# Kernel optimization log

Measured on AMD Instinct MI355X. Metric: run time of the kernel, lower is better.

Reference implementation:

```python
import jax, jax.numpy as jnp
import numpy as np

B, T, C, H = 8, 4096, 1024, 64

def setup_inputs() -> dict:
    key = jax.random.key(0)
    k1, k2, k3, k4 = jax.random.split(key, 4)
    return {
        "x": jax.random.normal(k1, (B, T, C), dtype=jnp.float32),
        "Wq": jax.random.normal(k2, (C, H), dtype=jnp.float32) * (C ** -0.5),
        "Wk": jax.random.normal(k3, (C, H), dtype=jnp.float32) * (C ** -0.5),
        "Wv": jax.random.normal(k4, (C, H), dtype=jnp.float32) * (C ** -0.5),
    }

def reference(x, Wq, Wk, Wv):
    # x: [B, T, C]; projections are bias-free Linears
    q = jnp.einsum("btc,ch->bth", x, Wq)  # [B, T, H]
    k = jnp.einsum("btc,ch->bth", x, Wk)
    v = jnp.einsum("btc,ch->bth", x, Wv)
    # NOTE: original scales by C**-0.5 (embed size), not head_size**-0.5
    scores = jnp.einsum("bqh,bkh->bqk", q, k) * (x.shape[-1] ** -0.5)  # [B, T, T]
    causal = jnp.tril(jnp.ones((x.shape[1], x.shape[1]), dtype=bool))
    scores = jnp.where(causal, scores, -jnp.inf)
    weights = jax.nn.softmax(scores, axis=-1)
    # dropout p=0.0 (eval) -> identity
    return jnp.einsum("bqk,bkh->bqh", weights, v)  # [B, T, H]
```

## Files before the change

### kernel.cpp

```cpp
#include <hip/hip_runtime.h>
#include <hip/hip_bf16.h>

typedef __attribute__((ext_vector_type(8))) short short8;
typedef __attribute__((ext_vector_type(4))) float f32x4;
typedef unsigned short u16;
typedef unsigned int u32;
typedef unsigned long long u64;

typedef u64    __attribute__((may_alias)) u64a;
typedef short8 __attribute__((may_alias)) short8a;
typedef float4 __attribute__((may_alias)) float4a;

#define Tseq 4096
#define LPP  72

__device__ __forceinline__ u32 pk_bf(float a, float b) {
    union { __hip_bfloat162 h; u32 u; } t;
    float2 f; f.x = a; f.y = b;
    t.h = __float22bfloat162_rn(f);
    return t.u;
}

__device__ __forceinline__ u16 f2bf(float f) {
    u32 u = __float_as_uint(f);
    u = (u + 0x7FFFu + ((u >> 16) & 1u)) >> 16;
    return (u16)u;
}

__device__ __forceinline__ short8 ld_frag_lds(const u16* p) {
    union { short8 v; u64 u[2]; } t;
    t.u[0] = *(const u64a*)(p);
    t.u[1] = *(const u64a*)(p + 4);
    return t.v;
}

__device__ __forceinline__ short8 cvt8(float4 a, float4 b) {
    union { short8 s; u32 u[4]; } t;
    t.u[0] = pk_bf(a.x, a.y); t.u[1] = pk_bf(a.z, a.w);
    t.u[2] = pk_bf(b.x, b.y); t.u[3] = pk_bf(b.z, b.w);
    return t.s;
}

__device__ __forceinline__ void gld_lds16(const void* g, void* l) {
    __builtin_amdgcn_global_load_lds(
        (const __attribute__((address_space(1))) u32*)g,
        (__attribute__((address_space(3))) u32*)l, 16, 0, 0);
}

__global__ __launch_bounds__(256) void wt_kernel(const float* __restrict__ Wq,
                                                 const float* __restrict__ Wk,
                                                 const float* __restrict__ Wv,
                                                 u16* __restrict__ wtf) {
    int idx = blockIdx.x * 256 + threadIdx.x;
    int lane = idx & 63, cc = (idx >> 6) & 31, n = (idx >> 11) & 3, mat = idx >> 13;
    const float* W = (mat == 0) ? Wq : ((mat == 1) ? Wk : Wv);
    float sc = (mat == 0) ? 0.03125f : 1.0f;
    int h = n * 16 + (lane & 15);
    int cbase = cc * 32 + (lane >> 4) * 8;
    union { short8 s; u32 u[4]; } t;
#pragma unroll
    for (int j2 = 0; j2 < 4; ++j2) {
        float a = W[(size_t)(cbase + j2 * 2)     * 64 + h] * sc;
        float b = W[(size_t)(cbase + j2 * 2 + 1) * 64 + h] * sc;
        t.u[j2] = pk_bf(a, b);
    }
    *(short8a*)(wtf + (size_t)idx * 8) = t.s;
}

__global__ __launch_bounds__(256, 2) void proj_kernel(const float* __restrict__ x,
                                                      const u16* __restrict__ wtf,
                                                      u16* __restrict__ qb,
                                                      u16* __restrict__ kA,
                                                      u16* __restrict__ vA) {
    __shared__ __align__(16) u16 Wl[2][12 * 2 * 64 * 8];

    const int tid = threadIdx.x, lane = tid & 63, wave = tid >> 6;
    const int m = lane & 15, quad = lane >> 4;
    const long rowbase = (long)blockIdx.x * 64 + wave * 16;
    const float* xr = x + (rowbase + m) * 1024 + quad * 8;

    f32x4 acc[12];
#pragma unroll
    for (int i = 0; i < 12; ++i) acc[i] = (f32x4){0.f, 0.f, 0.f, 0.f};

#define STAGE(p, buf)                                                          \
    {                                                                          \
        _Pragma("unroll")                                                      \
        for (int i = 0; i < 6; ++i) {                                          \
            int c = wave * 6 + i, mn = c >> 1, ccp = c & 1;                    \
            const u16* g = wtf + ((size_t)(mn * 32 + (p) * 2 + ccp) * 64 + lane) * 8; \
            u16* l = &Wl[buf][(size_t)(mn * 2 + ccp) * 512];                   \
            gld_lds16(g, l);                                                   \
        }                                                                      \
    }

    float4 xa[4], xb[4];
#pragma unroll
    for (int t = 0; t < 4; ++t)
        xa[t] = *(const float4a*)(xr + (t >> 1) * 32 + (t & 1) * 4);
#pragma unroll
    for (int t = 0; t < 4; ++t)
        xb[t] = *(const float4a*)(xr + (2 + (t >> 1)) * 32 + (t & 1) * 4);

    STAGE(0, 0);
    __syncthreads();

    for (int p = 0; p < 16; ++p) {
        if (p < 15) STAGE(p + 1, (p + 1) & 1);
        float4 xn[4];
        if (p < 14) {
#pragma unroll
            for (int t = 0; t < 4; ++t)
                xn[t] = *(const float4a*)(xr + (2 * (p + 2) + (t >> 1)) * 32 + (t & 1) * 4);
        }
        const u16* wb = Wl[p & 1];
#pragma unroll
        for (int ccp = 0; ccp < 2; ++ccp) {
            short8 af = cvt8(xa[ccp * 2], xa[ccp * 2 + 1]);
#pragma unroll
            for (int mn = 0; mn < 12; ++mn) {
                short8 bf = *(const short8a*)(wb + ((size_t)(mn * 2 + ccp) * 64 + lane) * 8);
                acc[mn] = __builtin_amdgcn_mfma_f32_16x16x32_bf16(af, bf, acc[mn], 0, 0, 0);
            }
        }
#pragma unroll
        for (int t = 0; t < 4; ++t) { xa[t] = xb[t]; if (p < 14) xb[t] = xn[t]; }
        __syncthreads();
    }
#undef STAGE

    const int b  = (int)(rowbase >> 12);
    const int tb = (int)(rowbase & 4095);

#pragma unroll
    for (int n = 0; n < 4; ++n)
#pragma unroll
        for (int r = 0; r < 4; ++r)
            qb[(rowbase + quad * 4 + r) * 64 + n * 16 + m] = f2bf(acc[n][r]);

#pragma unroll
    for (int n = 0; n < 4; ++n) {
        int kk = n >> 1;
        int lq = (n * 2 + (m >> 3)) & 3;
        int j  = m & 7;
#pragma unroll
        for (int r = 0; r < 4; ++r) {
            int key = tb + quad * 4 + r;
            size_t a = ((((size_t)b * 256 + (key >> 4)) * 2 + kk) * 64
                        + ((key & 15) + 16 * lq)) * 8 + j;
            kA[a] = f2bf(acc[4 + n][r]);
        }
    }

    {
        int key0 = tb + quad * 4;
        int j0 = key0 & 7;
        int q2 = (key0 >> 3) & 3;
        int kc = key0 >> 5;
#pragma unroll
        for (int n = 0; n < 4; ++n) {
            u64 pv = (u64)pk_bf(acc[8 + n][0], acc[8 + n][1])
                   | ((u64)pk_bf(acc[8 + n][2], acc[8 + n][3]) << 32);
            size_t a = ((((size_t)b * 4 + n) * 128 + kc) * 64 + (m + 16 * q2)) * 8 + j0;
            *(u64a*)(vA + a) = pv;
        }
    }
}

struct K8 { short8 k[8]; };

__device__ __forceinline__ void loadK(K8& f, const u16* kAb, int kt, int lane) {
    const u16* kp = kAb + (size_t)kt * 4096 + (size_t)lane * 8;
#pragma unroll
    for (int mt = 0; mt < 4; ++mt) {
        f.k[mt * 2]     = *(const short8a*)(kp + mt * 1024);
        f.k[mt * 2 + 1] = *(const short8a*)(kp + mt * 1024 + 512);
    }
}

__device__ __forceinline__ void attn_step(const K8& f, const u16* vAb,
        short8 qf0, short8 qf1, u16* pw,
        f32x4& o0, f32x4& o1, f32x4& o2, f32x4& o3,
        float& lsum, int kt, int n_s, int qrow, int quad, int m, int lane) {
    const float L2E = 1.4426950408889634f;
    const float FMB = 4.0f * L2E;
    const u16* vp = vAb + (size_t)kt * 1024 + (size_t)lane * 8;
    short8 vf[8];
#pragma unroll
    for (int ht = 0; ht < 4; ++ht) {
        vf[ht * 2]     = *(const short8a*)(vp + (size_t)ht * 65536);
        vf[ht * 2 + 1] = *(const short8a*)(vp + (size_t)ht * 65536 + 512);
    }
    f32x4 s[4];
#pragma unroll
    for (int mt = 0; mt < 4; ++mt) {
        f32x4 a = (f32x4){0.f, 0.f, 0.f, 0.f};
        a = __builtin_amdgcn_mfma_f32_16x16x32_bf16(f.k[mt * 2],     qf0, a, 0, 0, 0);
        a = __builtin_amdgcn_mfma_f32_16x16x32_bf16(f.k[mt * 2 + 1], qf1, a, 0, 0, 0);
        s[mt] = a;
    }
    if (kt == n_s) {
#pragma unroll
        for (int mt = 0; mt < 4; ++mt)
#pragma unroll
            for (int r = 0; r < 4; ++r) {
                int key = kt * 64 + mt * 16 + quad * 4 + r;
                if (key > qrow) s[mt][r] = -1e30f;
            }
    }
#pragma unroll
    for (int mt = 0; mt < 4; ++mt) {
        float p0 = __builtin_amdgcn_exp2f(s[mt][0] * L2E - FMB);
        float p1 = __builtin_amdgcn_exp2f(s[mt][1] * L2E - FMB);
        float p2 = __builtin_amdgcn_exp2f(s[mt][2] * L2E - FMB);
        float p3 = __builtin_amdgcn_exp2f(s[mt][3] * L2E - FMB);
        lsum += (p0 + p1) + (p2 + p3);
        u64 pv = (u64)pk_bf(p0, p1) | ((u64)pk_bf(p2, p3) << 32);
        *(u64a*)(pw + m * LPP + mt * 16 + quad * 4) = pv;
    }
    __builtin_amdgcn_wave_barrier();
    short8 pf0 = ld_frag_lds(pw + m * LPP + quad * 8);
    short8 pf1 = ld_frag_lds(pw + m * LPP + 32 + quad * 8);
    o0 = __builtin_amdgcn_mfma_f32_16x16x32_bf16(vf[0], pf0, o0, 0, 0, 0);
    o0 = __builtin_amdgcn_mfma_f32_16x16x32_bf16(vf[1], pf1, o0, 0, 0, 0);
    o1 = __builtin_amdgcn_mfma_f32_16x16x32_bf16(vf[2], pf0, o1, 0, 0, 0);
    o1 = __builtin_amdgcn_mfma_f32_16x16x32_bf16(vf[3], pf1, o1, 0, 0, 0);
    o2 = __builtin_amdgcn_mfma_f32_16x16x32_bf16(vf[4], pf0, o2, 0, 0, 0);
    o2 = __builtin_amdgcn_mfma_f32_16x16x32_bf16(vf[5], pf1, o2, 0, 0, 0);
    o3 = __builtin_amdgcn_mfma_f32_16x16x32_bf16(vf[6], pf0, o3, 0, 0, 0);
    o3 = __builtin_amdgcn_mfma_f32_16x16x32_bf16(vf[7], pf1, o3, 0, 0, 0);
}

__global__ __launch_bounds__(256, 3) void attn_kernel(const u16* __restrict__ qb,
                                                      const u16* __restrict__ kA,
                                                      const u16* __restrict__ vA,
                                                      float* __restrict__ out) {
    __shared__ __align__(16) u16 Pt[4][16 * LPP];
    __shared__ float Ob[2][16][64];
    __shared__ float Lb[2][64];

    const int tid = threadIdx.x, lane = tid & 63, wave = tid >> 6;
    const int m = lane & 15, quad = lane >> 4;
    const int beta = blockIdx.x;
    const int b = beta & 7, u = beta >> 3;
    const int role = (wave + beta) & 3;
    const int slot = role >> 1;
    const int half = role & 1;
    const int s = slot ? (255 - u) : u;
    const int qbase = s * 16;
    const int n_s = s >> 2;
    const int h = (n_s + 1) >> 1;
    const int kt0 = half ? h : 0;
    const int kt1 = half ? n_s : (h - 1);

    const u16* qp = qb + ((size_t)b * Tseq + qbase + m) * 64;
    short8 qf0 = *(const short8a*)(qp + quad * 8);
    short8 qf1 = *(const short8a*)(qp + 32 + quad * 8);

    const u16* kAb = kA + (size_t)b * (256 * 2 * 64 * 8);
    const u16* vAb = vA + (size_t)b * (4 * 128 * 64 * 8);
    u16* pw = Pt[wave];

    f32x4 o0 = {0.f, 0.f, 0.f, 0.f}, o1 = o0, o2 = o0, o3 = o0;
    float lsum = 0.f;
    const int qrow = qbase + m;

    if (kt0 <= kt1) {
        K8 ka, kb2;
        loadK(ka, kAb, kt0, lane);
        int kt = kt0;
        while (true) {
            if (kt < kt1) loadK(kb2, kAb, kt + 1, lane);
            attn_step(ka, vAb, qf0, qf1, pw, o0, o1, o2, o3, lsum,
                      kt, n_s, qrow, quad, m, lane);
            if (kt == kt1) break;
            ++kt;
            if (kt < kt1) loadK(ka, kAb, kt + 1, lane);
            attn_step(kb2, vAb, qf0, qf1, pw, o0, o1, o2, o3, lsum,
                      kt, n_s, qrow, quad, m, lane);
            if (kt == kt1) break;
            ++kt;
        }
    }

    if (half == 1) {
#pragma unroll
        for (int hn = 0; hn < 4; ++hn) {
            Ob[slot][hn * 4 + 0][lane] = o0[hn];
        }
        Ob[slot][0][lane] = o0[0]; Ob[slot][1][lane] = o0[1];
        Ob[slot][2][lane] = o0[2]; Ob[slot][3][lane] = o0[3];
        Ob[slot][4][lane] = o1[0]; Ob[slot][5][lane] = o1[1];
        Ob[slot][6][lane] = o1[2]; Ob[slot][7][lane] = o1[3];
        Ob[slot][8][lane] = o2[0]; Ob[slot][9][lane] = o2[1];
        Ob[slot][10][lane] = o2[2]; Ob[slot][11][lane] = o2[3];
        Ob[slot][12][lane] = o3[0]; Ob[slot][13][lane] = o3[1];
        Ob[slot][14][lane] = o3[2]; Ob[slot][15][lane] = o3[3];
        Lb[slot][lane] = lsum;
    }
    __syncthreads();
    if (half == 0) {
        o0[0] += Ob[slot][0][lane]; o0[1] += Ob[slot][1][lane];
        o0[2] += Ob[slot][2][lane]; o0[3] += Ob[slot][3][lane];
        o1[0] += Ob[slot][4][lane]; o1[1] += Ob[slot][5][lane];
        o1[2] += Ob[slot][6][lane]; o1[3] += Ob[slot][7][lane];
        o2[0] += Ob[slot][8][lane]; o2[1] += Ob[slot][9][lane];
        o2[2] += Ob[slot][10][lane]; o2[3] += Ob[slot][11][lane];
        o3[0] += Ob[slot][12][lane]; o3[1] += Ob[slot][13][lane];
        o3[2] += Ob[slot][14][lane]; o3[3] += Ob[slot][15][lane];
        lsum += Lb[slot][lane];

        lsum += __shfl_xor(lsum, 16, 64);
        lsum += __shfl_xor(lsum, 32, 64);
        float inv = 1.0f / lsum;

        float* orow = out + ((size_t)b * Tseq + qbase + m) * 64;
        float4 w;
        w.x = o0[0] * inv; w.y = o0[1] * inv; w.z = o0[2] * inv; w.w = o0[3] * inv;
        *(float4a*)(orow + 0 * 16 + quad * 4) = w;
        w.x = o1[0] * inv; w.y = o1[1] * inv; w.z = o1[2] * inv; w.w = o1[3] * inv;
        *(float4a*)(orow + 1 * 16 + quad * 4) = w;
        w.x = o2[0] * inv; w.y = o2[1] * inv; w.z = o2[2] * inv; w.w = o2[3] * inv;
        *(float4a*)(orow + 2 * 16 + quad * 4) = w;
        w.x = o3[0] * inv; w.y = o3[1] * inv; w.z = o3[2] * inv; w.w = o3[3] * inv;
        *(float4a*)(orow + 3 * 16 + quad * 4) = w;
    }
}

extern "C" void kernel_launch(void* const* d_in, const int* in_sizes, int n_in,
                              void* d_out, int out_size, void* d_ws, size_t ws_size,
                              hipStream_t stream) {
    const float* x  = (const float*)d_in[0];
    const float* Wq = (const float*)d_in[1];
    const float* Wk = (const float*)d_in[2];
    const float* Wv = (const float*)d_in[3];
    float* out = (float*)d_out;

    char* ws = (char*)d_ws;
    u16* wtf = (u16*)ws;
    u16* qb  = (u16*)(ws + 512 * 1024);
    u16* kA  = (u16*)(ws + 512 * 1024 + 4 * 1024 * 1024);
    u16* vA  = (u16*)(ws + 512 * 1024 + 8 * 1024 * 1024);

    wt_kernel<<<96, 256, 0, stream>>>(Wq, Wk, Wv, wtf);
    proj_kernel<<<512, 256, 0, stream>>>(x, wtf, qb, kA, vA);
    attn_kernel<<<1024, 256, 0, stream>>>(qb, kA, vA, out);
}
```

Before: 252.2 us.

## Double per-wave row tiles in projection and attention to reuse K/V and W fragments

The projection kernel now handles 128 rows per block, two 16-row strips per wave, so each LDS weight fragment feeds two MFMAs. The attention kernel is restructured so each wave processes 32 query rows (two 16-row tiles) against each loaded K/V tile, with 8 waves per block and a 4-way pairing of tiles for causal load balance. Both changes halve the global/LDS fragment loads per unit of MFMA work but raise register pressure, drop the K double-buffer prefetch, and leave fewer blocks to fill the GPU.

```diff
diff --git a/kernel.cpp b/kernel.cpp
--- a/kernel.cpp
+++ b/kernel.cpp
@@ -67,21 +67,25 @@
     *(short8a*)(wtf + (size_t)idx * 8) = t.s;
 }
 
-__global__ __launch_bounds__(256, 2) void proj_kernel(const float* __restrict__ x,
-                                                      const u16* __restrict__ wtf,
-                                                      u16* __restrict__ qb,
-                                                      u16* __restrict__ kA,
-                                                      u16* __restrict__ vA) {
+__global__ __launch_bounds__(256) void proj_kernel(const float* __restrict__ x,
+                                                   const u16* __restrict__ wtf,
+                                                   u16* __restrict__ qb,
+                                                   u16* __restrict__ kA,
+                                                   u16* __restrict__ vA) {
     __shared__ __align__(16) u16 Wl[2][12 * 2 * 64 * 8];
 
     const int tid = threadIdx.x, lane = tid & 63, wave = tid >> 6;
     const int m = lane & 15, quad = lane >> 4;
-    const long rowbase = (long)blockIdx.x * 64 + wave * 16;
-    const float* xr = x + (rowbase + m) * 1024 + quad * 8;
-
-    f32x4 acc[12];
-#pragma unroll
-    for (int i = 0; i < 12; ++i) acc[i] = (f32x4){0.f, 0.f, 0.f, 0.f};
+    const long rowA = (long)blockIdx.x * 128 + wave * 16;
+    const float* xrA = x + (rowA + m) * 1024 + quad * 8;
+    const float* xrB = xrA + 64 * 1024;
+
+    f32x4 accA[12], accB[12];
+#pragma unroll
+    for (int i = 0; i < 12; ++i) {
+        accA[i] = (f32x4){0.f, 0.f, 0.f, 0.f};
+        accB[i] = (f32x4){0.f, 0.f, 0.f, 0.f};
+    }
 
 #define STAGE(p, buf)                                                          \
     {                                                                          \
@@ -94,236 +98,253 @@
         }                                                                      \
     }
 
-    float4 xa[4], xb[4];
-#pragma unroll
-    for (int t = 0; t < 4; ++t)
-        xa[t] = *(const float4a*)(xr + (t >> 1) * 32 + (t & 1) * 4);
-#pragma unroll
-    for (int t = 0; t < 4; ++t)
-        xb[t] = *(const float4a*)(xr + (2 + (t >> 1)) * 32 + (t & 1) * 4);
+    float4 xa[8], xb[8];
+#pragma unroll
+    for (int t = 0; t < 8; ++t) {
+        const float* base = (t < 4) ? xrA : xrB;
+        int tt = t & 3;
+        xa[t] = *(const float4a*)(base + ((tt >> 1)) * 32 + (tt & 1) * 4);
+        xb[t] = *(const float4a*)(base + (2 + (tt >> 1)) * 32 + (tt & 1) * 4);
+    }
 
     STAGE(0, 0);
     __syncthreads();
 
     for (int p = 0; p < 16; ++p) {
         if (p < 15) STAGE(p + 1, (p + 1) & 1);
-        float4 xn[4];
+        float4 xn[8];
         if (p < 14) {
 #pragma unroll
-            for (int t = 0; t < 4; ++t)
-                xn[t] = *(const float4a*)(xr + (2 * (p + 2) + (t >> 1)) * 32 + (t & 1) * 4);
+            for (int t = 0; t < 8; ++t) {
+                const float* base = (t < 4) ? xrA : xrB;
+                int tt = t & 3;
+                xn[t] = *(const float4a*)(base + (2 * (p + 2) + (tt >> 1)) * 32 + (tt & 1) * 4);
+            }
         }
         const u16* wb = Wl[p & 1];
 #pragma unroll
         for (int ccp = 0; ccp < 2; ++ccp) {
-            short8 af = cvt8(xa[ccp * 2], xa[ccp * 2 + 1]);
+            short8 afA = cvt8(xa[ccp * 2], xa[ccp * 2 + 1]);
+            short8 afB = cvt8(xa[4 + ccp * 2], xa[4 + ccp * 2 + 1]);
 #pragma unroll
             for (int mn = 0; mn < 12; ++mn) {
                 short8 bf = *(const short8a*)(wb + ((size_t)(mn * 2 + ccp) * 64 + lane) * 8);
-                acc[mn] = __builtin_amdgcn_mfma_f32_16x16x32_bf16(af, bf, acc[mn], 0, 0, 0);
-            }
-        }
-#pragma unroll
-        for (int t = 0; t < 4; ++t) { xa[t] = xb[t]; if (p < 14) xb[t] = xn[t]; }
+                accA[mn] = __builtin_amdgcn_mfma_f32_16x16x32_bf16(afA, bf, accA[mn], 0, 0, 0);
+                accB[mn] = __builtin_amdgcn_mfma_f32_16x16x32_bf16(afB, bf, accB[mn], 0, 0, 0);
+            }
+        }
+#pragma unroll
+        for (int t = 0; t < 8; ++t) { xa[t] = xb[t]; if (p < 14) xb[t] = xn[t]; }
         __syncthreads();
     }
 #undef STAGE
 
-    const int b  = (int)(rowbase >> 12);
-    const int tb = (int)(rowbase & 4095);
-
-#pragma unroll
-    for (int n = 0; n < 4; ++n)
-#pragma unroll
-        for (int r = 0; r < 4; ++r)
-            qb[(rowbase + quad * 4 + r) * 64 + n * 16 + m] = f2bf(acc[n][r]);
-
-#pragma unroll
-    for (int n = 0; n < 4; ++n) {
-        int kk = n >> 1;
-        int lq = (n * 2 + (m >> 3)) & 3;
-        int j  = m & 7;
-#pragma unroll
-        for (int r = 0; r < 4; ++r) {
-            int key = tb + quad * 4 + r;
-            size_t a = ((((size_t)b * 256 + (key >> 4)) * 2 + kk) * 64
-                        + ((key & 15) + 16 * lq)) * 8 + j;
-            kA[a] = f2bf(acc[4 + n][r]);
-        }
-    }
-
-    {
-        int key0 = tb + quad * 4;
-        int j0 = key0 & 7;
-        int q2 = (key0 >> 3) & 3;
-        int kc = key0 >> 5;
+#pragma unroll
+    for (int strip = 0; strip < 2; ++strip) {
+        const f32x4* acc = strip ? accB : accA;
+        long rowbase = rowA + strip * 64;
+        int b  = (int)(rowbase >> 12);
+        int tb = (int)(rowbase & 4095);
+
+#pragma unroll
+        for (int n = 0; n < 4; ++n)
+#pragma unroll
+            for (int r = 0; r < 4; ++r)
+                qb[(rowbase + quad * 4 + r) * 64 + n * 16 + m] = f2bf(acc[n][r]);
+
 #pragma unroll
         for (int n = 0; n < 4; ++n) {
-            u64 pv = (u64)pk_bf(acc[8 + n][0], acc[8 + n][1])
-                   | ((u64)pk_bf(acc[8 + n][2], acc[8 + n][3]) << 32);
-            size_t a = ((((size_t)b * 4 + n) * 128 + kc) * 64 + (m + 16 * q2)) * 8 + j0;
-            *(u64a*)(vA + a) = pv;
-        }
-    }
-}
-
-struct K8 { short8 k[8]; };
-
-__device__ __forceinline__ void loadK(K8& f, const u16* kAb, int kt, int lane) {
-    const u16* kp = kAb + (size_t)kt * 4096 + (size_t)lane * 8;
-#pragma unroll
-    for (int mt = 0; mt < 4; ++mt) {
-        f.k[mt * 2]     = *(const short8a*)(kp + mt * 1024);
-        f.k[mt * 2 + 1] = *(const short8a*)(kp + mt * 1024 + 512);
-    }
-}
-
-__device__ __forceinline__ void attn_step(const K8& f, const u16* vAb,
-        short8 qf0, short8 qf1, u16* pw,
-        f32x4& o0, f32x4& o1, f32x4& o2, f32x4& o3,
-        float& lsum, int kt, int n_s, int qrow, int quad, int m, int lane) {
+            int kk = n >> 1;
+            int lq = (n * 2 + (m >> 3)) & 3;
+            int j  = m & 7;
+#pragma unroll
+            for (int r = 0; r < 4; ++r) {
+                int key = tb + quad * 4 + r;
+                size_t a = ((((size_t)b * 256 + (key >> 4)) * 2 + kk) * 64
+                            + ((key & 15) + 16 * lq)) * 8 + j;
+                kA[a] = f2bf(acc[4 + n][r]);
+            }
+        }
+
+        {
+            int key0 = tb + quad * 4;
+            int j0 = key0 & 7;
+            int q2 = (key0 >> 3) & 3;
+            int kc = key0 >> 5;
+#pragma unroll
+            for (int n = 0; n < 4; ++n) {
+                u64 pv = (u64)pk_bf(acc[8 + n][0], acc[8 + n][1])
+                       | ((u64)pk_bf(acc[8 + n][2], acc[8 + n][3]) << 32);
+                size_t a = ((((size_t)b * 4 + n) * 128 + kc) * 64 + (m + 16 * q2)) * 8 + j0;
+                *(u64a*)(vA + a) = pv;
+            }
+        }
+    }
+}
+
+__global__ __launch_bounds__(512) void attn_kernel(const u16* __restrict__ qb,
+                                                   const u16* __restrict__ kA,
+                                                   const u16* __restrict__ vA,
+                                                   float* __restrict__ out) {
+    __shared__ __align__(16) u16 Pt[8][2][16 * LPP];
+    __shared__ float MO[4][2][16][64];
+    __shared__ float ML[4][2][64];
+
+    const int tid = threadIdx.x, lane = tid & 63, wave = tid >> 6;
+    const int m = lane & 15, quad = lane >> 4;
+    const int b = blockIdx.x & 7, g = blockIdx.x >> 3;
+    const int pi = wave >> 1, half = wave & 1;
+
+    int t;
+    if      (pi == 0) t = 2 * g;
+    else if (pi == 1) t = 127 - 2 * g;
+    else if (pi == 2) t = 2 * g + 1;
+    else              t = 126 - 2 * g;
+
+    const int qbase = t * 32;
+    const int n_t = t >> 1;
+    const int h = (n_t + 1) >> 1;
+    const int kt0 = half ? h : 0;
+    const int kt1 = half ? n_t : (h - 1);
+
+    const u16* qpA = qb + ((size_t)b * Tseq + qbase + m) * 64;
+    const u16* qpB = qpA + 16 * 64;
+    short8 qfA0 = *(const short8a*)(qpA + quad * 8);
+    short8 qfA1 = *(const short8a*)(qpA + 32 + quad * 8);
+    short8 qfB0 = *(const short8a*)(qpB + quad * 8);
+    short8 qfB1 = *(const short8a*)(qpB + 32 + quad * 8);
+
+    const u16* kAb = kA + (size_t)b * (256 * 2 * 64 * 8);
+    const u16* vAb = vA + (size_t)b * (4 * 128 * 64 * 8);
+    u16* pwA = Pt[wave][0];
+    u16* pwB = Pt[wave][1];
+
+    f32x4 oA[4], oB[4];
+#pragma unroll
+    for (int i = 0; i < 4; ++i) {
+        oA[i] = (f32x4){0.f, 0.f, 0.f, 0.f};
+        oB[i] = (f32x4){0.f, 0.f, 0.f, 0.f};
+    }
+    float lsA = 0.f, lsB = 0.f;
+    const int qrowA = qbase + m, qrowB = qbase + 16 + m;
     const float L2E = 1.4426950408889634f;
     const float FMB = 4.0f * L2E;
-    const u16* vp = vAb + (size_t)kt * 1024 + (size_t)lane * 8;
-    short8 vf[8];
-#pragma unroll
-    for (int ht = 0; ht < 4; ++ht) {
-        vf[ht * 2]     = *(const short8a*)(vp + (size_t)ht * 65536);
-        vf[ht * 2 + 1] = *(const short8a*)(vp + (size_t)ht * 65536 + 512);
-    }
-    f32x4 s[4];
-#pragma unroll
-    for (int mt = 0; mt < 4; ++mt) {
-        f32x4 a = (f32x4){0.f, 0.f, 0.f, 0.f};
-        a = __builtin_amdgcn_mfma_f32_16x16x32_bf16(f.k[mt * 2],     qf0, a, 0, 0, 0);
-        a = __builtin_amdgcn_mfma_f32_16x16x32_bf16(f.k[mt * 2 + 1], qf1, a, 0, 0, 0);
-        s[mt] = a;
-    }
-    if (kt == n_s) {
-#pragma unroll
-        for (int mt = 0; mt < 4; ++mt)
+
+    for (int kt = kt0; kt <= kt1; ++kt) {
+        const u16* kp = kAb + (size_t)kt * 4096 + (size_t)lane * 8;
+        short8 kf[8];
+#pragma unroll
+        for (int mt = 0; mt < 4; ++mt) {
+            kf[mt * 2]     = *(const short8a*)(kp + mt * 1024);
+            kf[mt * 2 + 1] = *(const short8a*)(kp + mt * 1024 + 512);
+        }
+        const u16* vp = vAb + (size_t)kt * 1024 + (size_t)lane * 8;
+        short8 vf[8];
+#pragma unroll
+        for (int ht = 0; ht < 4; ++ht) {
+            vf[ht * 2]     = *(const short8a*)(vp + (size_t)ht * 65536);
+            vf[ht * 2 + 1] = *(const short8a*)(vp + (size_t)ht * 65536 + 512);
+        }
+
+        f32x4 sA[4], sB[4];
+#pragma unroll
+        for (int mt = 0; mt < 4; ++mt) {
+            f32x4 a = (f32x4){0.f, 0.f, 0.f, 0.f};
+            a = __builtin_amdgcn_mfma_f32_16x16x32_bf16(kf[mt * 2],     qfA0, a, 0, 0, 0);
+            a = __builtin_amdgcn_mfma_f32_16x16x32_bf16(kf[mt * 2 + 1], qfA1, a, 0, 0, 0);
+            sA[mt] = a;
+            f32x4 c = (f32x4){0.f, 0.f, 0.f, 0.f};
+            c = __builtin_amdgcn_mfma_f32_16x16x32_bf16(kf[mt * 2],     qfB0, c, 0, 0, 0);
+            c = __builtin_amdgcn_mfma_f32_16x16x32_bf16(kf[mt * 2 + 1], qfB1, c, 0, 0, 0);
+            sB[mt] = c;
+        }
+
+        if (kt == n_t) {
+#pragma unroll
+            for (int mt = 0; mt < 4; ++mt)
+#pragma unroll
+                for (int r = 0; r < 4; ++r) {
+                    int key = kt * 64 + mt * 16 + quad * 4 + r;
+                    if (key > qrowA) sA[mt][r] = -1e30f;
+                    if (key > qrowB) sB[mt][r] = -1e30f;
+                }
+        }
+
+#pragma unroll
+        for (int mt = 0; mt < 4; ++mt) {
+            float a0 = __builtin_amdgcn_exp2f(sA[mt][0] * L2E - FMB);
+            float a1 = __builtin_amdgcn_exp2f(sA[mt][1] * L2E - FMB);
+            float a2 = __builtin_amdgcn_exp2f(sA[mt][2] * L2E - FMB);
+            float a3 = __builtin_amdgcn_exp2f(sA[mt][3] * L2E - FMB);
+            lsA += (a0 + a1) + (a2 + a3);
+            *(u64a*)(pwA + m * LPP + mt * 16 + quad * 4) =
+                (u64)pk_bf(a0, a1) | ((u64)pk_bf(a2, a3) << 32);
+            float b0 = __builtin_amdgcn_exp2f(sB[mt][0] * L2E - FMB);
+            float b1 = __builtin_amdgcn_exp2f(sB[mt][1] * L2E - FMB);
+            float b2 = __builtin_amdgcn_exp2f(sB[mt][2] * L2E - FMB);
+            float b3 = __builtin_amdgcn_exp2f(sB[mt][3] * L2E - FMB);
+            lsB += (b0 + b1) + (b2 + b3);
+            *(u64a*)(pwB + m * LPP + mt * 16 + quad * 4) =
+                (u64)pk_bf(b0, b1) | ((u64)pk_bf(b2, b3) << 32);
+        }
+
+        short8 pA0 = ld_frag_lds(pwA + m * LPP + quad * 8);
+        short8 pA1 = ld_frag_lds(pwA + m * LPP + 32 + quad * 8);
+        short8 pB0 = ld_frag_lds(pwB + m * LPP + quad * 8);
+        short8 pB1 = ld_frag_lds(pwB + m * LPP + 32 + quad * 8);
+
+#pragma unroll
+        for (int hn = 0; hn < 4; ++hn) {
+            oA[hn] = __builtin_amdgcn_mfma_f32_16x16x32_bf16(vf[hn * 2],     pA0, oA[hn], 0, 0, 0);
+            oA[hn] = __builtin_amdgcn_mfma_f32_16x16x32_bf16(vf[hn * 2 + 1], pA1, oA[hn], 0, 0, 0);
+            oB[hn] = __builtin_amdgcn_mfma_f32_16x16x32_bf16(vf[hn * 2],     pB0, oB[hn], 0, 0, 0);
+            oB[hn] = __builtin_amdgcn_mfma_f32_16x16x32_bf16(vf[hn * 2 + 1], pB1, oB[hn], 0, 0, 0);
+        }
+    }
+
+    if (half == 1) {
+#pragma unroll
+        for (int j = 0; j < 4; ++j) {
 #pragma unroll
             for (int r = 0; r < 4; ++r) {
-                int key = kt * 64 + mt * 16 + quad * 4 + r;
-                if (key > qrow) s[mt][r] = -1e30f;
-            }
-    }
-#pragma unroll
-    for (int mt = 0; mt < 4; ++mt) {
-        float p0 = __builtin_amdgcn_exp2f(s[mt][0] * L2E - FMB);
-        float p1 = __builtin_amdgcn_exp2f(s[mt][1] * L2E - FMB);
-        float p2 = __builtin_amdgcn_exp2f(s[mt][2] * L2E - FMB);
-        float p3 = __builtin_amdgcn_exp2f(s[mt][3] * L2E - FMB);
-        lsum += (p0 + p1) + (p2 + p3);
-        u64 pv = (u64)pk_bf(p0, p1) | ((u64)pk_bf(p2, p3) << 32);
-        *(u64a*)(pw + m * LPP + mt * 16 + quad * 4) = pv;
-    }
-    __builtin_amdgcn_wave_barrier();
-    short8 pf0 = ld_frag_lds(pw + m * LPP + quad * 8);
-    short8 pf1 = ld_frag_lds(pw + m * LPP + 32 + quad * 8);
-    o0 = __builtin_amdgcn_mfma_f32_16x16x32_bf16(vf[0], pf0, o0, 0, 0, 0);
-    o0 = __builtin_amdgcn_mfma_f32_16x16x32_bf16(vf[1], pf1, o0, 0, 0, 0);
-    o1 = __builtin_amdgcn_mfma_f32_16x16x32_bf16(vf[2], pf0, o1, 0, 0, 0);
-    o1 = __builtin_amdgcn_mfma_f32_16x16x32_bf16(vf[3], pf1, o1, 0, 0, 0);
-    o2 = __builtin_amdgcn_mfma_f32_16x16x32_bf16(vf[4], pf0, o2, 0, 0, 0);
-    o2 = __builtin_amdgcn_mfma_f32_16x16x32_bf16(vf[5], pf1, o2, 0, 0, 0);
-    o3 = __builtin_amdgcn_mfma_f32_16x16x32_bf16(vf[6], pf0, o3, 0, 0, 0);
-    o3 = __builtin_amdgcn_mfma_f32_16x16x32_bf16(vf[7], pf1, o3, 0, 0, 0);
-}
-
-__global__ __launch_bounds__(256, 3) void attn_kernel(const u16* __restrict__ qb,
-                                                      const u16* __restrict__ kA,
-                                                      const u16* __restrict__ vA,
-                                                      float* __restrict__ out) {
-    __shared__ __align__(16) u16 Pt[4][16 * LPP];
-    __shared__ float Ob[2][16][64];
-    __shared__ float Lb[2][64];
-
-    const int tid = threadIdx.x, lane = tid & 63, wave = tid >> 6;
-    const int m = lane & 15, quad = lane >> 4;
-    const int beta = blockIdx.x;
-    const int b = beta & 7, u = beta >> 3;
-    const int role = (wave + beta) & 3;
-    const int slot = role >> 1;
-    const int half = role & 1;
-    const int s = slot ? (255 - u) : u;
-    const int qbase = s * 16;
-    const int n_s = s >> 2;
-    const int h = (n_s + 1) >> 1;
-    const int kt0 = half ? h : 0;
-    const int kt1 = half ? n_s : (h - 1);
-
-    const u16* qp = qb + ((size_t)b * Tseq + qbase + m) * 64;
-    short8 qf0 = *(const short8a*)(qp + quad * 8);
-    short8 qf1 = *(const short8a*)(qp + 32 + quad * 8);
-
-    const u16* kAb = kA + (size_t)b * (256 * 2 * 64 * 8);
-    const u16* vAb = vA + (size_t)b * (4 * 128 * 64 * 8);
-    u16* pw = Pt[wave];
-
-    f32x4 o0 = {0.f, 0.f, 0.f, 0.f}, o1 = o0, o2 = o0, o3 = o0;
-    float lsum = 0.f;
-    const int qrow = qbase + m;
-
-    if (kt0 <= kt1) {
-        K8 ka, kb2;
-        loadK(ka, kAb, kt0, lane);
-        int kt = kt0;
-        while (true) {
-            if (kt < kt1) loadK(kb2, kAb, kt + 1, lane);
-            attn_step(ka, vAb, qf0, qf1, pw, o0, o1, o2, o3, lsum,
-                      kt, n_s, qrow, quad, m, lane);
-            if (kt == kt1) break;
-            ++kt;
-            if (kt < kt1) loadK(ka, kAb, kt + 1, lane);
-            attn_step(kb2, vAb, qf0, qf1, pw, o0, o1, o2, o3, lsum,
-                      kt, n_s, qrow, quad, m, lane);
-            if (kt == kt1) break;
-            ++kt;
-        }
-    }
-
-    if (half == 1) {
-#pragma unroll
-        for (int hn = 0; hn < 4; ++hn) {
-            Ob[slot][hn * 4 + 0][lane] = o0[hn];
-        }
-        Ob[slot][0][lane] = o0[0]; Ob[slot][1][lane] = o0[1];
-        Ob[slot][2][lane] = o0[2]; Ob[slot][3][lane] = o0[3];
-        Ob[slot][4][lane] = o1[0]; Ob[slot][5][lane] = o1[1];
-        Ob[slot][6][lane] = o1[2]; Ob[slot][7][lane] = o1[3];
-        Ob[slot][8][lane] = o2[0]; Ob[slot][9][lane] = o2[1];
-        Ob[slot][10][lane] = o2[2]; Ob[slot][11][lane] = o2[3];
-        Ob[slot][12][lane] = o3[0]; Ob[slot][13][lane] = o3[1];
-        Ob[slot][14][lane] = o3[2]; Ob[slot][15][lane] = o3[3];
-        Lb[slot][lane] = lsum;
+                MO[pi][0][j * 4 + r][lane] = oA[j][r];
+                MO[pi][1][j * 4 + r][lane] = oB[j][r];
+            }
+        }
+        ML[pi][0][lane] = lsA;
+        ML[pi][1][lane] = lsB;
     }
     __syncthreads();
     if (half == 0) {
-        o0[0] += Ob[slot][0][lane]; o0[1] += Ob[slot][1][lane];
-        o0[2] += Ob[slot][2][lane]; o0[3] += Ob[slot][3][lane];
-        o1[0] += Ob[slot][4][lane]; o1[1] += Ob[slot][5][lane];
-        o1[2] += Ob[slot][6][lane]; o1[3] += Ob[slot][7][lane];
-        o2[0] += Ob[slot][8][lane]; o2[1] += Ob[slot][9][lane];
-        o2[2] += Ob[slot][10][lane]; o2[3] += Ob[slot][11][lane];
-        o3[0] += Ob[slot][12][lane]; o3[1] += Ob[slot][13][lane];
-        o3[2] += Ob[slot][14][lane]; o3[3] += Ob[slot][15][lane];
-        lsum += Lb[slot][lane];
-
-        lsum += __shfl_xor(lsum, 16, 64);
-        lsum += __shfl_xor(lsum, 32, 64);
-        float inv = 1.0f / lsum;
-
-        float* orow = out + ((size_t)b * Tseq + qbase + m) * 64;
+#pragma unroll
+        for (int j = 0; j < 4; ++j) {
+#pragma unroll
+            for (int r = 0; r < 4; ++r) {
+                oA[j][r] += MO[pi][0][j * 4 + r][lane];
+                oB[j][r] += MO[pi][1][j * 4 + r][lane];
+            }
+        }
+        lsA += ML[pi][0][lane];
+        lsB += ML[pi][1][lane];
+
+        lsA += __shfl_xor(lsA, 16, 64);
+        lsA += __shfl_xor(lsA, 32, 64);
+        lsB += __shfl_xor(lsB, 16, 64);
+        lsB += __shfl_xor(lsB, 32, 64);
+        float invA = 1.0f / lsA, invB = 1.0f / lsB;
+
+        float* orA = out + ((size_t)b * Tseq + qbase + m) * 64;
+        float* orB = orA + 16 * 64;
         float4 w;
-        w.x = o0[0] * inv; w.y = o0[1] * inv; w.z = o0[2] * inv; w.w = o0[3] * inv;
-        *(float4a*)(orow + 0 * 16 + quad * 4) = w;
-        w.x = o1[0] * inv; w.y = o1[1] * inv; w.z = o1[2] * inv; w.w = o1[3] * inv;
-        *(float4a*)(orow + 1 * 16 + quad * 4) = w;
-        w.x = o2[0] * inv; w.y = o2[1] * inv; w.z = o2[2] * inv; w.w = o2[3] * inv;
-        *(float4a*)(orow + 2 * 16 + quad * 4) = w;
-        w.x = o3[0] * inv; w.y = o3[1] * inv; w.z = o3[2] * inv; w.w = o3[3] * inv;
-        *(float4a*)(orow + 3 * 16 + quad * 4) = w;
+#pragma unroll
+        for (int hn = 0; hn < 4; ++hn) {
+            w.x = oA[hn][0] * invA; w.y = oA[hn][1] * invA;
+            w.z = oA[hn][2] * invA; w.w = oA[hn][3] * invA;
+            *(float4a*)(orA + hn * 16 + quad * 4) = w;
+            w.x = oB[hn][0] * invB; w.y = oB[hn][1] * invB;
+            w.z = oB[hn][2] * invB; w.w = oB[hn][3] * invB;
+            *(float4a*)(orB + hn * 16 + quad * 4) = w;
+        }
     }
 }
 
@@ -343,6 +364,6 @@
     u16* vA  = (u16*)(ws + 512 * 1024 + 8 * 1024 * 1024);
 
     wt_kernel<<<96, 256, 0, stream>>>(Wq, Wk, Wv, wtf);
-    proj_kernel<<<512, 256, 0, stream>>>(x, wtf, qb, kA, vA);
-    attn_kernel<<<1024, 256, 0, stream>>>(qb, kA, vA, out);
-}
+    proj_kernel<<<256, 256, 0, stream>>>(x, wtf, qb, kA, vA);
+    attn_kernel<<<256, 512, 0, stream>>>(qb, kA, vA, out);
+}
```

New measurement: 264.0 us. 1.05x slower.
